# Kernel optimization log

Measured on AMD Instinct MI355X. Metric: run time of the kernel, lower is better.

The kernel has to match this reference:

```python
import jax, jax.numpy as jnp
import numpy as np

GAMMA = 0.7
ALPHA = 1.0
EPS = 1e-6

def setup_inputs() -> dict:
    key = jax.random.key(0)
    k1, k2 = jax.random.split(key)
    x = jax.random.normal(k1, (1, 4096, 1024), dtype=jnp.float32)
    attn = jax.random.uniform(k2, (1, 4096, 4096), dtype=jnp.float32)
    return {"x": x, "attn": attn, "layer_idx": 10, "total_layers": 12}


def reference(x, attn, layer_idx, total_layers):
    B, N, D = x.shape  # module's masking/cat logic requires B == 1
    if layer_idx < GAMMA * total_layers:
        return x

    # --- spatial autocorrelation score s ---
    a = x.mean(axis=-1)                                            # [B,N]
    z = (a - a.mean(1, keepdims=True)) / (a.std(1, ddof=1, keepdims=True) + EPS)
    # diag(z z^T * W) == z^2 * diag(W): skip the O(N^2) outer product
    I_l = z * z * jnp.diagonal(attn, axis1=-2, axis2=-1)           # [B,N]
    s = (I_l - I_l.mean(1, keepdims=True)) / (I_l.std(1, ddof=1, keepdims=True) + EPS)

    # --- threshold (torch.median returns the LOWER middle for even N) ---
    mu_s = s.mean(1, keepdims=True)
    abs_med = jnp.sort(jnp.abs(s), axis=1)[:, (N - 1) // 2][:, None]
    lb = ALPHA * (mu_s - abs_med)
    ub = ALPHA * (mu_s + abs_med)
    mask_A = (s < lb) | (s > ub)                                   # [B,N]

    xb = x[0]
    mA = mask_A[0]
    idx = jnp.arange(N)
    n_A = mA.sum()

    # compact A tokens to the front preserving original order
    orderA = jnp.argsort(~mA, stable=True)
    tokA = xb[orderA]                    # first n_A rows are tokens_A, rest are B tokens (masked later)
    mid = n_A // 2
    n2 = n_A - mid                       # number of A2 tokens

    # A1[i] = tokA[i] (valid i < mid); A2[j] = tokA[mid + j] (valid j < n2)
    A2 = jnp.take(tokA, jnp.clip(mid + idx, 0, N - 1), axis=0)     # [N,D] padded
    validA1 = idx < mid
    validA2 = idx < n2

    sim = tokA @ A2.T                                              # [N,N]
    sim = jnp.where(validA2[None, :], sim, -jnp.inf)
    matches = jnp.argmax(sim, axis=1)                              # [N]
    merged = 0.5 * (tokA + A2[matches])
    merged = jnp.where(validA1[:, None], merged, 0.0)              # rows >= mid zeroed

    # residual A2 tokens (not matched by any valid A1 row), compacted and zero-padded
    drop_idx = jnp.where(validA1, matches, N)                      # OOB index dropped
    matched = jnp.zeros(N, bool).at[drop_idx].set(True, mode='drop')
    resid_valid = validA2 & ~matched
    orderR = jnp.argsort(~resid_valid, stable=True)
    residual = jnp.where(resid_valid[orderR][:, None], A2[orderR], 0.0)  # [N,D]

    # B tokens compacted, then merged tokens appended, zero pad to N
    n_B = N - n_A
    orderB = jnp.argsort(mA, stable=True)
    tokB = jnp.where((idx < n_B)[:, None], xb[orderB], 0.0)        # [N,D]
    shift = jnp.clip(idx - n_B, 0, N - 1)
    in_merged = ((idx >= n_B) & (idx < n_B + mid)).astype(xb.dtype)[:, None]
    out = (tokB + in_merged * merged[shift])[None]                 # [1,N,D]
    return out, residual
```

## Files before the change

### kernel.cpp

```cpp
#include <hip/hip_runtime.h>

#define N 4096
#define D 1024
#define EPSF 1e-6f

typedef _Float16 f16;
typedef f16 f16x8 __attribute__((ext_vector_type(8)));
typedef float f32x4 __attribute__((ext_vector_type(4)));
typedef unsigned long long u64;

struct WS {
  int n_A, mid, n2, n_B, n_resid, pad[3];
  float a[N];
  int A1idx[N];
  int A2idx[N];
  int Bidx[N];
  int matches[N];
  int residIdx[N];
  u64 bestKey[2048];
};

__device__ __forceinline__ u64 packKey(float v, int j) {
  unsigned u = __float_as_uint(v);
  unsigned m = (u & 0x80000000u) ? ~u : (u | 0x80000000u);
  return ((u64)m << 32) | (unsigned)(~(unsigned)j);
}

__global__ __launch_bounds__(256) void k_prep(const float* __restrict__ x, WS* ws) {
  int row = blockIdx.x;
  int t = threadIdx.x;
  float4 v = ((const float4*)(x + (size_t)row * D))[t];
  float sm = v.x + v.y + v.z + v.w;
  for (int o = 32; o; o >>= 1) sm += __shfl_down(sm, o, 64);
  __shared__ float w[4];
  if ((t & 63) == 0) w[t >> 6] = sm;
  __syncthreads();
  if (t == 0) ws->a[row] = (w[0] + w[1] + w[2] + w[3]) * (1.0f / D);
}

__global__ __launch_bounds__(1024) void k_mask(const float* __restrict__ attn, WS* ws) {
  __shared__ double dred[16], dred2[16];
  __shared__ float bcast[2];
  __shared__ int hist[256];
  __shared__ int wsum[16];
  __shared__ unsigned sPrefix;
  __shared__ int sRank;
  int tid = threadIdx.x;
  int lane = tid & 63, wv = tid >> 6;

  ws->bestKey[tid] = 0ull;
  ws->bestKey[tid + 1024] = 0ull;

  float av[4];
  double s = 0.0, s2 = 0.0;
  #pragma unroll
  for (int q = 0; q < 4; q++) {
    float f = ws->a[tid * 4 + q];
    av[q] = f; s += f; s2 += (double)f * f;
  }
  for (int o = 32; o; o >>= 1) { s += __shfl_down(s, o, 64); s2 += __shfl_down(s2, o, 64); }
  if (lane == 0) { dred[wv] = s; dred2[wv] = s2; }
  __syncthreads();
  if (tid == 0) {
    double t1 = 0, t2 = 0;
    for (int i = 0; i < 16; i++) { t1 += dred[i]; t2 += dred2[i]; }
    bcast[0] = (float)(t1 / N);
    bcast[1] = (float)sqrt((t2 - t1 * t1 / N) / (N - 1));
  }
  __syncthreads();
  float meanA = bcast[0], stdA = bcast[1];

  float il[4];
  s = 0.0; s2 = 0.0;
  #pragma unroll
  for (int q = 0; q < 4; q++) {
    int i = tid * 4 + q;
    float z = (av[q] - meanA) / (stdA + EPSF);
    float I = z * z * attn[(size_t)i * N + i];
    il[q] = I; s += I; s2 += (double)I * I;
  }
  for (int o = 32; o; o >>= 1) { s += __shfl_down(s, o, 64); s2 += __shfl_down(s2, o, 64); }
  __syncthreads();
  if (lane == 0) { dred[wv] = s; dred2[wv] = s2; }
  __syncthreads();
  if (tid == 0) {
    double t1 = 0, t2 = 0;
    for (int i = 0; i < 16; i++) { t1 += dred[i]; t2 += dred2[i]; }
    bcast[0] = (float)(t1 / N);
    bcast[1] = (float)sqrt((t2 - t1 * t1 / N) / (N - 1));
    sPrefix = 0u; sRank = (N - 1) / 2;
  }
  __syncthreads();
  float meanI = bcast[0], stdI = bcast[1];

  float sv[4]; unsigned ab[4];
  #pragma unroll
  for (int q = 0; q < 4; q++) {
    float sval = (il[q] - meanI) / (stdI + EPSF);
    sv[q] = sval;
    ab[q] = __float_as_uint(fabsf(sval));
  }

  for (int p = 3; p >= 0; p--) {
    if (tid < 256) hist[tid] = 0;
    __syncthreads();
    unsigned pre = sPrefix;
    int rk = sRank;
    int sh = p * 8;
    unsigned mHi = (p == 3) ? 0u : (0xFFFFFFFFu << (sh + 8));
    #pragma unroll
    for (int q = 0; q < 4; q++)
      if ((ab[q] & mHi) == pre) atomicAdd(&hist[(ab[q] >> sh) & 255], 1);
    __syncthreads();
    int v = (tid < 256) ? hist[tid] : 0;
    int inc = v;
    #pragma unroll
    for (int o = 1; o < 64; o <<= 1) { int u = __shfl_up(inc, o, 64); if (lane >= o) inc += u; }
    if (lane == 63) wsum[wv] = inc;
    __syncthreads();
    if (tid < 16) {
      int t = wsum[tid];
      #pragma unroll
      for (int o = 1; o < 16; o <<= 1) { int u = __shfl_up(t, o, 64); if (tid >= o) t += u; }
      wsum[tid] = t;
    }
    __syncthreads();
    int incl = (wv ? wsum[wv - 1] : 0) + inc;
    int E = incl - v;
    if (tid < 256 && v && rk >= E && rk < E + v) {
      sPrefix = pre | ((unsigned)tid << sh);
      sRank = rk - E;
    }
    __syncthreads();
  }
  float med = __uint_as_float(sPrefix);

  int msk[4], loc[4]; int tot = 0;
  #pragma unroll
  for (int q = 0; q < 4; q++) {
    bool m = fabsf(sv[q]) > med;
    msk[q] = m; loc[q] = tot; tot += (int)m;
  }
  int inc = tot;
  #pragma unroll
  for (int o = 1; o < 64; o <<= 1) { int u = __shfl_up(inc, o, 64); if (lane >= o) inc += u; }
  if (lane == 63) wsum[wv] = inc;
  __syncthreads();
  if (tid < 16) {
    int t = wsum[tid];
    #pragma unroll
    for (int o = 1; o < 16; o <<= 1) { int u = __shfl_up(t, o, 64); if (tid >= o) t += u; }
    wsum[tid] = t;
  }
  __syncthreads();
  int nA = wsum[15];
  int base = (wv ? wsum[wv - 1] : 0) + inc - tot;
  int midl = nA >> 1;
  #pragma unroll
  for (int q = 0; q < 4; q++) {
    int i = tid * 4 + q;
    int r = base + loc[q];
    if (msk[q]) {
      if (r < midl) ws->A1idx[r] = i; else ws->A2idx[r - midl] = i;
    } else {
      ws->Bidx[i - r] = i;
    }
  }
  if (tid == 0) { ws->n_A = nA; ws->mid = midl; ws->n2 = nA - midl; ws->n_B = N - nA; }
}

__global__ __launch_bounds__(256) void k_gemm(const float* __restrict__ x, WS* ws) {
  const int mid = ws->mid, n2 = ws->n2;
  const int bi = blockIdx.y, bj = blockIdx.x;
  if (bi * 64 >= mid || bj * 64 >= n2) return;

  __shared__ f16 lds[2][4][64 * 64];

  const int tid = threadIdx.x;
  const int lane = tid & 63;
  const int wid = tid >> 6;
  const int wr = wid >> 1, wc = wid & 1;

  const int srow = tid >> 2;
  const int sc = tid & 3;
  int ra = bi * 64 + srow; if (ra > mid - 1) ra = mid - 1;
  int rb = bj * 64 + srow; if (rb > n2 - 1) rb = n2 - 1;
  const float* pA = x + (size_t)ws->A1idx[ra] * D;
  const float* pB = x + (size_t)ws->A2idx[rb] * D;

  const int wo0 = srow * 64 + (((sc * 2) ^ (srow & 7)) * 8);
  const int wo1 = srow * 64 + (((sc * 2 + 1) ^ (srow & 7)) * 8);

  float fav[16], fbv[16];
  auto LOAD = [&](int t) {
    const float4* qa = (const float4*)(pA + t * 64 + sc * 16);
    const float4* qb = (const float4*)(pB + t * 64 + sc * 16);
    #pragma unroll
    for (int q = 0; q < 4; q++) {
      float4 va = qa[q], vb = qb[q];
      fav[q * 4 + 0] = va.x; fav[q * 4 + 1] = va.y; fav[q * 4 + 2] = va.z; fav[q * 4 + 3] = va.w;
      fbv[q * 4 + 0] = vb.x; fbv[q * 4 + 1] = vb.y; fbv[q * 4 + 2] = vb.z; fbv[q * 4 + 3] = vb.w;
    }
  };
  auto STORE = [&](int buf) {
    f16x8 ah0, ah1, al0, al1, bh0, bh1, bl0, bl1;
    #pragma unroll
    for (int e = 0; e < 8; e++) {
      f16 h;
      h = (f16)fav[e];     ah0[e] = h; al0[e] = (f16)(fav[e] - (float)h);
      h = (f16)fav[8 + e]; ah1[e] = h; al1[e] = (f16)(fav[8 + e] - (float)h);
      h = (f16)fbv[e];     bh0[e] = h; bl0[e] = (f16)(fbv[e] - (float)h);
      h = (f16)fbv[8 + e]; bh1[e] = h; bl1[e] = (f16)(fbv[8 + e] - (float)h);
    }
    *(f16x8*)&lds[buf][0][wo0] = ah0; *(f16x8*)&lds[buf][0][wo1] = ah1;
    *(f16x8*)&lds[buf][1][wo0] = al0; *(f16x8*)&lds[buf][1][wo1] = al1;
    *(f16x8*)&lds[buf][2][wo0] = bh0; *(f16x8*)&lds[buf][2][wo1] = bh1;
    *(f16x8*)&lds[buf][3][wo0] = bl0; *(f16x8*)&lds[buf][3][wo1] = bl1;
  };

  const int colg = lane & 15, rowg = lane >> 4;
  const int ma0 = wr * 32 + colg, ma1 = ma0 + 16;
  const int mb0 = wc * 32 + colg, mb1 = mb0 + 16;

  f32x4 zero = {0.0f, 0.0f, 0.0f, 0.0f};
  f32x4 acc[2][2];
  acc[0][0] = zero; acc[0][1] = zero; acc[1][0] = zero; acc[1][1] = zero;

#define FRAG(buf, t4, row, g) \
  (*(const f16x8*)&lds[buf][t4][(row) * 64 + ((((g) ^ ((row) & 7))) * 8)])

  LOAD(0);
  STORE(0);
  __syncthreads();
  for (int t16 = 0; t16 < 16; t16++) {
    int buf = t16 & 1;
    if (t16 < 15) LOAD(t16 + 1);
    #pragma unroll
    for (int ks = 0; ks < 2; ks++) {
      int gk = ks * 4 + rowg;
      f16x8 ah0 = FRAG(buf, 0, ma0, gk), ah1 = FRAG(buf, 0, ma1, gk);
      f16x8 al0 = FRAG(buf, 1, ma0, gk), al1 = FRAG(buf, 1, ma1, gk);
      f16x8 bh0 = FRAG(buf, 2, mb0, gk), bh1 = FRAG(buf, 2, mb1, gk);
      f16x8 bl0 = FRAG(buf, 3, mb0, gk), bl1 = FRAG(buf, 3, mb1, gk);
      acc[0][0] = __builtin_amdgcn_mfma_f32_16x16x32_f16(ah0, bh0, acc[0][0], 0, 0, 0);
      acc[0][0] = __builtin_amdgcn_mfma_f32_16x16x32_f16(ah0, bl0, acc[0][0], 0, 0, 0);
      acc[0][0] = __builtin_amdgcn_mfma_f32_16x16x32_f16(al0, bh0, acc[0][0], 0, 0, 0);
      acc[0][1] = __builtin_amdgcn_mfma_f32_16x16x32_f16(ah0, bh1, acc[0][1], 0, 0, 0);
      acc[0][1] = __builtin_amdgcn_mfma_f32_16x16x32_f16(ah0, bl1, acc[0][1], 0, 0, 0);
      acc[0][1] = __builtin_amdgcn_mfma_f32_16x16x32_f16(al0, bh1, acc[0][1], 0, 0, 0);
      acc[1][0] = __builtin_amdgcn_mfma_f32_16x16x32_f16(ah1, bh0, acc[1][0], 0, 0, 0);
      acc[1][0] = __builtin_amdgcn_mfma_f32_16x16x32_f16(ah1, bl0, acc[1][0], 0, 0, 0);
      acc[1][0] = __builtin_amdgcn_mfma_f32_16x16x32_f16(al1, bh0, acc[1][0], 0, 0, 0);
      acc[1][1] = __builtin_amdgcn_mfma_f32_16x16x32_f16(ah1, bh1, acc[1][1], 0, 0, 0);
      acc[1][1] = __builtin_amdgcn_mfma_f32_16x16x32_f16(ah1, bl1, acc[1][1], 0, 0, 0);
      acc[1][1] = __builtin_amdgcn_mfma_f32_16x16x32_f16(al1, bh1, acc[1][1], 0, 0, 0);
    }
    if (t16 < 15) {
      __syncthreads();
      STORE(buf ^ 1);
      __syncthreads();
    }
  }
#undef FRAG

  #pragma unroll
  for (int mi = 0; mi < 2; mi++) {
    #pragma unroll
    for (int i = 0; i < 4; i++) {
      int grow = bi * 64 + wr * 32 + mi * 16 + rowg * 4 + i;
      u64 key = 0;
      #pragma unroll
      for (int ni = 0; ni < 2; ni++) {
        int gcol = bj * 64 + wc * 32 + ni * 16 + colg;
        if (gcol < n2) {
          u64 k2 = packKey(acc[mi][ni][i], gcol);
          if (k2 > key) key = k2;
        }
      }
      #pragma unroll
      for (int m = 8; m; m >>= 1) {
        u64 o = (u64)__shfl_xor((long long)key, m, 64);
        if (o > key) key = o;
      }
      if (colg == 0 && grow < mid) atomicMax(&ws->bestKey[grow], key);
    }
  }
}

__global__ __launch_bounds__(1024) void k_match(WS* ws) {
  __shared__ int flag[N];
  __shared__ int wsum[16];
  int tid = threadIdx.x;
  int lane = tid & 63, wv = tid >> 6;
  int mid = ws->mid, n2 = ws->n2;
  #pragma unroll
  for (int q = 0; q < 4; q++) flag[tid * 4 + q] = 0;
  __syncthreads();
  #pragma unroll
  for (int q = 0; q < 2; q++) {
    int r = tid + q * 1024;
    if (r < mid) {
      int j = (int)(~(unsigned)(ws->bestKey[r] & 0xffffffffull));
      ws->matches[r] = j;
      flag[j] = 1;
    }
  }
  __syncthreads();
  int v[4], loc[4]; int tot = 0;
  #pragma unroll
  for (int q = 0; q < 4; q++) {
    int j = tid * 4 + q;
    bool val = (j < n2) && (flag[j] == 0);
    v[q] = val; loc[q] = tot; tot += (int)val;
  }
  int inc = tot;
  #pragma unroll
  for (int o = 1; o < 64; o <<= 1) { int u = __shfl_up(inc, o, 64); if (lane >= o) inc += u; }
  if (lane == 63) wsum[wv] = inc;
  __syncthreads();
  if (tid < 16) {
    int t = wsum[tid];
    #pragma unroll
    for (int o = 1; o < 16; o <<= 1) { int u = __shfl_up(t, o, 64); if (tid >= o) t += u; }
    wsum[tid] = t;
  }
  __syncthreads();
  int base = (wv ? wsum[wv - 1] : 0) + inc - tot;
  #pragma unroll
  for (int q = 0; q < 4; q++)
    if (v[q]) ws->residIdx[base + loc[q]] = ws->A2idx[tid * 4 + q];
  if (tid == 0) ws->n_resid = wsum[15];
}

__global__ __launch_bounds__(256) void k_write(const float* __restrict__ x,
                                               float* __restrict__ out, WS* ws) {
  int r = blockIdx.x;
  int t = threadIdx.x;
  int n_B = ws->n_B, mid = ws->mid, n_resid = ws->n_resid;
  float4 res = make_float4(0.f, 0.f, 0.f, 0.f);
  if (r < N) {
    if (r < n_B) {
      res = ((const float4*)(x + (size_t)ws->Bidx[r] * D))[t];
    } else if (r < n_B + mid) {
      int m = r - n_B;
      float4 v1 = ((const float4*)(x + (size_t)ws->A1idx[m] * D))[t];
      float4 v2 = ((const float4*)(x + (size_t)ws->A2idx[ws->matches[m]] * D))[t];
      res = make_float4(0.5f * (v1.x + v2.x), 0.5f * (v1.y + v2.y),
                        0.5f * (v1.z + v2.z), 0.5f * (v1.w + v2.w));
    }
  } else {
    int k = r - N;
    if (k < n_resid) {
      res = ((const float4*)(x + (size_t)ws->residIdx[k] * D))[t];
    }
  }
  ((float4*)(out + (size_t)r * D))[t] = res;
}

extern "C" void kernel_launch(void* const* d_in, const int* in_sizes, int n_in,
                              void* d_out, int out_size, void* d_ws, size_t ws_size,
                              hipStream_t stream) {
  const float* x = (const float*)d_in[0];
  const float* attn = (const float*)d_in[1];
  float* out = (float*)d_out;
  WS* ws = (WS*)d_ws;

  k_prep<<<N, 256, 0, stream>>>(x, ws);
  k_mask<<<1, 1024, 0, stream>>>(attn, ws);
  dim3 g(32, 32);
  k_gemm<<<g, 256, 0, stream>>>(x, ws);
  k_match<<<1, 1024, 0, stream>>>(ws);
  k_write<<<2 * N, 256, 0, stream>>>(x, out, ws);
}
```

Measured before the change: 68.93 us.

## Precompute fp16 hi/lo split in prep and use split-K direct-load GEMM

The prep kernel now writes fp16 hi/lo splits of x into the output buffer, used as scratch. The GEMM no longer converts fp32 to fp16 pairs per tile through LDS. The GEMM switches to 32x32 tiles with two waves, each covering half of K. Fragments load directly from global memory without LDS staging, the two halves are combined through shared memory, and blocks are remapped with an XCD-aware swizzle. This removes repeated conversion work and LDS barriers but gives up LDS reuse, relying on cache for the repeated row reads. It also depends on k_write later overwriting the scratch region of the output.

Result: slower. 74.05 us (+7.4%).

```diff
diff --git a/kernel.cpp b/kernel.cpp
--- a/kernel.cpp
+++ b/kernel.cpp
@@ -6,6 +6,7 @@
 
 typedef _Float16 f16;
 typedef f16 f16x8 __attribute__((ext_vector_type(8)));
+typedef f16 f16x4 __attribute__((ext_vector_type(4)));
 typedef float f32x4 __attribute__((ext_vector_type(4)));
 typedef unsigned long long u64;
 
@@ -26,10 +27,22 @@
   return ((u64)m << 32) | (unsigned)(~(unsigned)j);
 }
 
-__global__ __launch_bounds__(256) void k_prep(const float* __restrict__ x, WS* ws) {
+__global__ __launch_bounds__(256) void k_prep(const float* __restrict__ x,
+                                              f16* __restrict__ hi,
+                                              f16* __restrict__ lo, WS* ws) {
   int row = blockIdx.x;
   int t = threadIdx.x;
   float4 v = ((const float4*)(x + (size_t)row * D))[t];
+  float vv[4] = {v.x, v.y, v.z, v.w};
+  f16x4 h, l;
+  #pragma unroll
+  for (int q = 0; q < 4; q++) {
+    f16 hq = (f16)vv[q];
+    h[q] = hq;
+    l[q] = (f16)(vv[q] - (float)hq);
+  }
+  *(f16x4*)(hi + (size_t)row * D + t * 4) = h;
+  *(f16x4*)(lo + (size_t)row * D + t * 4) = l;
   float sm = v.x + v.y + v.z + v.w;
   for (int o = 32; o; o >>= 1) sm += __shfl_down(sm, o, 64);
   __shared__ float w[4];
@@ -169,120 +182,111 @@
   if (tid == 0) { ws->n_A = nA; ws->mid = midl; ws->n2 = nA - midl; ws->n_B = N - nA; }
 }
 
-__global__ __launch_bounds__(256) void k_gemm(const float* __restrict__ x, WS* ws) {
+__global__ __launch_bounds__(128) void k_gemm(const f16* __restrict__ hi,
+                                              const f16* __restrict__ lo, WS* ws) {
   const int mid = ws->mid, n2 = ws->n2;
-  const int bi = blockIdx.y, bj = blockIdx.x;
-  if (bi * 64 >= mid || bj * 64 >= n2) return;
-
-  __shared__ f16 lds[2][4][64 * 64];
+  int L = blockIdx.x;
+  int local = L >> 3;
+  int bj = ((L & 7) << 2) | (local >> 5);
+  int bi = local & 31;
+  if (bi * 32 >= mid || bj * 32 >= n2) return;
+
+  __shared__ float comb[64][17];
 
   const int tid = threadIdx.x;
+  const int w = tid >> 6;
   const int lane = tid & 63;
-  const int wid = tid >> 6;
-  const int wr = wid >> 1, wc = wid & 1;
-
-  const int srow = tid >> 2;
-  const int sc = tid & 3;
-  int ra = bi * 64 + srow; if (ra > mid - 1) ra = mid - 1;
-  int rb = bj * 64 + srow; if (rb > n2 - 1) rb = n2 - 1;
-  const float* pA = x + (size_t)ws->A1idx[ra] * D;
-  const float* pB = x + (size_t)ws->A2idx[rb] * D;
-
-  const int wo0 = srow * 64 + (((sc * 2) ^ (srow & 7)) * 8);
-  const int wo1 = srow * 64 + (((sc * 2 + 1) ^ (srow & 7)) * 8);
-
-  float fav[16], fbv[16];
-  auto LOAD = [&](int t) {
-    const float4* qa = (const float4*)(pA + t * 64 + sc * 16);
-    const float4* qb = (const float4*)(pB + t * 64 + sc * 16);
-    #pragma unroll
-    for (int q = 0; q < 4; q++) {
-      float4 va = qa[q], vb = qb[q];
-      fav[q * 4 + 0] = va.x; fav[q * 4 + 1] = va.y; fav[q * 4 + 2] = va.z; fav[q * 4 + 3] = va.w;
-      fbv[q * 4 + 0] = vb.x; fbv[q * 4 + 1] = vb.y; fbv[q * 4 + 2] = vb.z; fbv[q * 4 + 3] = vb.w;
-    }
-  };
-  auto STORE = [&](int buf) {
-    f16x8 ah0, ah1, al0, al1, bh0, bh1, bl0, bl1;
-    #pragma unroll
-    for (int e = 0; e < 8; e++) {
-      f16 h;
-      h = (f16)fav[e];     ah0[e] = h; al0[e] = (f16)(fav[e] - (float)h);
-      h = (f16)fav[8 + e]; ah1[e] = h; al1[e] = (f16)(fav[8 + e] - (float)h);
-      h = (f16)fbv[e];     bh0[e] = h; bl0[e] = (f16)(fbv[e] - (float)h);
-      h = (f16)fbv[8 + e]; bh1[e] = h; bl1[e] = (f16)(fbv[8 + e] - (float)h);
-    }
-    *(f16x8*)&lds[buf][0][wo0] = ah0; *(f16x8*)&lds[buf][0][wo1] = ah1;
-    *(f16x8*)&lds[buf][1][wo0] = al0; *(f16x8*)&lds[buf][1][wo1] = al1;
-    *(f16x8*)&lds[buf][2][wo0] = bh0; *(f16x8*)&lds[buf][2][wo1] = bh1;
-    *(f16x8*)&lds[buf][3][wo0] = bl0; *(f16x8*)&lds[buf][3][wo1] = bl1;
-  };
-
   const int colg = lane & 15, rowg = lane >> 4;
-  const int ma0 = wr * 32 + colg, ma1 = ma0 + 16;
-  const int mb0 = wc * 32 + colg, mb1 = mb0 + 16;
-
-  f32x4 zero = {0.0f, 0.0f, 0.0f, 0.0f};
-  f32x4 acc[2][2];
-  acc[0][0] = zero; acc[0][1] = zero; acc[1][0] = zero; acc[1][1] = zero;
-
-#define FRAG(buf, t4, row, g) \
-  (*(const f16x8*)&lds[buf][t4][(row) * 64 + ((((g) ^ ((row) & 7))) * 8)])
-
-  LOAD(0);
-  STORE(0);
-  __syncthreads();
-  for (int t16 = 0; t16 < 16; t16++) {
-    int buf = t16 & 1;
-    if (t16 < 15) LOAD(t16 + 1);
-    #pragma unroll
-    for (int ks = 0; ks < 2; ks++) {
-      int gk = ks * 4 + rowg;
-      f16x8 ah0 = FRAG(buf, 0, ma0, gk), ah1 = FRAG(buf, 0, ma1, gk);
-      f16x8 al0 = FRAG(buf, 1, ma0, gk), al1 = FRAG(buf, 1, ma1, gk);
-      f16x8 bh0 = FRAG(buf, 2, mb0, gk), bh1 = FRAG(buf, 2, mb1, gk);
-      f16x8 bl0 = FRAG(buf, 3, mb0, gk), bl1 = FRAG(buf, 3, mb1, gk);
-      acc[0][0] = __builtin_amdgcn_mfma_f32_16x16x32_f16(ah0, bh0, acc[0][0], 0, 0, 0);
-      acc[0][0] = __builtin_amdgcn_mfma_f32_16x16x32_f16(ah0, bl0, acc[0][0], 0, 0, 0);
-      acc[0][0] = __builtin_amdgcn_mfma_f32_16x16x32_f16(al0, bh0, acc[0][0], 0, 0, 0);
-      acc[0][1] = __builtin_amdgcn_mfma_f32_16x16x32_f16(ah0, bh1, acc[0][1], 0, 0, 0);
-      acc[0][1] = __builtin_amdgcn_mfma_f32_16x16x32_f16(ah0, bl1, acc[0][1], 0, 0, 0);
-      acc[0][1] = __builtin_amdgcn_mfma_f32_16x16x32_f16(al0, bh1, acc[0][1], 0, 0, 0);
-      acc[1][0] = __builtin_amdgcn_mfma_f32_16x16x32_f16(ah1, bh0, acc[1][0], 0, 0, 0);
-      acc[1][0] = __builtin_amdgcn_mfma_f32_16x16x32_f16(ah1, bl0, acc[1][0], 0, 0, 0);
-      acc[1][0] = __builtin_amdgcn_mfma_f32_16x16x32_f16(al1, bh0, acc[1][0], 0, 0, 0);
-      acc[1][1] = __builtin_amdgcn_mfma_f32_16x16x32_f16(ah1, bh1, acc[1][1], 0, 0, 0);
-      acc[1][1] = __builtin_amdgcn_mfma_f32_16x16x32_f16(ah1, bl1, acc[1][1], 0, 0, 0);
-      acc[1][1] = __builtin_amdgcn_mfma_f32_16x16x32_f16(al1, bh1, acc[1][1], 0, 0, 0);
-    }
-    if (t16 < 15) {
-      __syncthreads();
-      STORE(buf ^ 1);
-      __syncthreads();
-    }
-  }
-#undef FRAG
-
-  #pragma unroll
-  for (int mi = 0; mi < 2; mi++) {
-    #pragma unroll
-    for (int i = 0; i < 4; i++) {
-      int grow = bi * 64 + wr * 32 + mi * 16 + rowg * 4 + i;
-      u64 key = 0;
+
+  int ar0 = bi * 32 + colg;      if (ar0 > mid - 1) ar0 = mid - 1;
+  int ar1 = ar0 + 16;            if (ar1 > mid - 1) ar1 = mid - 1;
+  int br0 = bj * 32 + colg;      if (br0 > n2 - 1) br0 = n2 - 1;
+  int br1 = br0 + 16;            if (br1 > n2 - 1) br1 = n2 - 1;
+  const size_t off = (size_t)w * 1024 + rowg * 16;
+  const char* pAh0 = (const char*)hi + (size_t)ws->A1idx[ar0] * 2048 + off;
+  const char* pAh1 = (const char*)hi + (size_t)ws->A1idx[ar1] * 2048 + off;
+  const char* pAl0 = (const char*)lo + (size_t)ws->A1idx[ar0] * 2048 + off;
+  const char* pAl1 = (const char*)lo + (size_t)ws->A1idx[ar1] * 2048 + off;
+  const char* pBh0 = (const char*)hi + (size_t)ws->A2idx[br0] * 2048 + off;
+  const char* pBh1 = (const char*)hi + (size_t)ws->A2idx[br1] * 2048 + off;
+  const char* pBl0 = (const char*)lo + (size_t)ws->A2idx[br0] * 2048 + off;
+  const char* pBl1 = (const char*)lo + (size_t)ws->A2idx[br1] * 2048 + off;
+
+  f32x4 zero = {0.f, 0.f, 0.f, 0.f};
+  f32x4 hh[2][2], hl[2][2], lh[2][2];
+  #pragma unroll
+  for (int i = 0; i < 2; i++)
+    #pragma unroll
+    for (int j = 0; j < 2; j++) { hh[i][j] = zero; hl[i][j] = zero; lh[i][j] = zero; }
+
+  #pragma unroll
+  for (int t = 0; t < 16; t++) {
+    const int o = t * 64;
+    f16x8 ah0 = *(const f16x8*)(pAh0 + o);
+    f16x8 ah1 = *(const f16x8*)(pAh1 + o);
+    f16x8 al0 = *(const f16x8*)(pAl0 + o);
+    f16x8 al1 = *(const f16x8*)(pAl1 + o);
+    f16x8 bh0 = *(const f16x8*)(pBh0 + o);
+    f16x8 bh1 = *(const f16x8*)(pBh1 + o);
+    f16x8 bl0 = *(const f16x8*)(pBl0 + o);
+    f16x8 bl1 = *(const f16x8*)(pBl1 + o);
+    hh[0][0] = __builtin_amdgcn_mfma_f32_16x16x32_f16(ah0, bh0, hh[0][0], 0, 0, 0);
+    hh[0][1] = __builtin_amdgcn_mfma_f32_16x16x32_f16(ah0, bh1, hh[0][1], 0, 0, 0);
+    hh[1][0] = __builtin_amdgcn_mfma_f32_16x16x32_f16(ah1, bh0, hh[1][0], 0, 0, 0);
+    hh[1][1] = __builtin_amdgcn_mfma_f32_16x16x32_f16(ah1, bh1, hh[1][1], 0, 0, 0);
+    hl[0][0] = __builtin_amdgcn_mfma_f32_16x16x32_f16(ah0, bl0, hl[0][0], 0, 0, 0);
+    hl[0][1] = __builtin_amdgcn_mfma_f32_16x16x32_f16(ah0, bl1, hl[0][1], 0, 0, 0);
+    hl[1][0] = __builtin_amdgcn_mfma_f32_16x16x32_f16(ah1, bl0, hl[1][0], 0, 0, 0);
+    hl[1][1] = __builtin_amdgcn_mfma_f32_16x16x32_f16(ah1, bl1, hl[1][1], 0, 0, 0);
+    lh[0][0] = __builtin_amdgcn_mfma_f32_16x16x32_f16(al0, bh0, lh[0][0], 0, 0, 0);
+    lh[0][1] = __builtin_amdgcn_mfma_f32_16x16x32_f16(al0, bh1, lh[0][1], 0, 0, 0);
+    lh[1][0] = __builtin_amdgcn_mfma_f32_16x16x32_f16(al1, bh0, lh[1][0], 0, 0, 0);
+    lh[1][1] = __builtin_amdgcn_mfma_f32_16x16x32_f16(al1, bh1, lh[1][1], 0, 0, 0);
+  }
+
+  f32x4 s[2][2];
+  #pragma unroll
+  for (int i = 0; i < 2; i++)
+    #pragma unroll
+    for (int j = 0; j < 2; j++) s[i][j] = (hh[i][j] + hl[i][j]) + lh[i][j];
+
+  if (w == 1) {
+    #pragma unroll
+    for (int i = 0; i < 2; i++)
       #pragma unroll
-      for (int ni = 0; ni < 2; ni++) {
-        int gcol = bj * 64 + wc * 32 + ni * 16 + colg;
-        if (gcol < n2) {
-          u64 k2 = packKey(acc[mi][ni][i], gcol);
-          if (k2 > key) key = k2;
+      for (int j = 0; j < 2; j++)
+        #pragma unroll
+        for (int r = 0; r < 4; r++) comb[lane][i * 8 + j * 4 + r] = s[i][j][r];
+  }
+  __syncthreads();
+  if (w == 0) {
+    #pragma unroll
+    for (int i = 0; i < 2; i++)
+      #pragma unroll
+      for (int j = 0; j < 2; j++)
+        #pragma unroll
+        for (int r = 0; r < 4; r++) s[i][j][r] += comb[lane][i * 8 + j * 4 + r];
+    #pragma unroll
+    for (int mi = 0; mi < 2; mi++) {
+      #pragma unroll
+      for (int r = 0; r < 4; r++) {
+        int grow = bi * 32 + mi * 16 + rowg * 4 + r;
+        u64 key = 0;
+        #pragma unroll
+        for (int ni = 0; ni < 2; ni++) {
+          int gcol = bj * 32 + ni * 16 + colg;
+          if (gcol < n2) {
+            u64 k2 = packKey(s[mi][ni][r], gcol);
+            if (k2 > key) key = k2;
+          }
         }
+        #pragma unroll
+        for (int m = 8; m; m >>= 1) {
+          u64 o = (u64)__shfl_xor((long long)key, m, 64);
+          if (o > key) key = o;
+        }
+        if (colg == 0 && grow < mid && key) atomicMax(&ws->bestKey[grow], key);
       }
-      #pragma unroll
-      for (int m = 8; m; m >>= 1) {
-        u64 o = (u64)__shfl_xor((long long)key, m, 64);
-        if (o > key) key = o;
-      }
-      if (colg == 0 && grow < mid) atomicMax(&ws->bestKey[grow], key);
     }
   }
 }
@@ -364,11 +368,12 @@
   const float* attn = (const float*)d_in[1];
   float* out = (float*)d_out;
   WS* ws = (WS*)d_ws;
-
-  k_prep<<<N, 256, 0, stream>>>(x, ws);
+  f16* hi = (f16*)d_out;
+  f16* lo = hi + (size_t)N * D;
+
+  k_prep<<<N, 256, 0, stream>>>(x, hi, lo, ws);
   k_mask<<<1, 1024, 0, stream>>>(attn, ws);
-  dim3 g(32, 32);
-  k_gemm<<<g, 256, 0, stream>>>(x, ws);
+  k_gemm<<<1024, 128, 0, stream>>>(hi, lo, ws);
   k_match<<<1, 1024, 0, stream>>>(ws);
   k_write<<<2 * N, 256, 0, stream>>>(x, out, ws);
 }
```

## Pre-pack gathered A tokens into fp16 hi/lo planes before GEMM

Applied to the files above, without the earlier changes.

Adds a k_pack kernel that gathers the A1/A2 rows and splits them once into fp16 hi and lo planes, stored in scratch space borrowed from the output buffer. The GEMM then loads the pre-split fp16 tiles straight into shared memory with one plane per wave, so the fp32 loads and hi/lo conversion are no longer repeated for every tile pair. The grid is also remapped to a swizzled 1D order, presumably to improve cache locality, and atomics with empty keys are skipped. The cost is an extra kernel launch plus writing and re-reading about 16 MB of packed data, and correctness depends on k_write overwriting the borrowed output region afterwards.

Result: faster. 64.07 us (-7.1%).

```diff
diff --git a/kernel.cpp b/kernel.cpp
--- a/kernel.cpp
+++ b/kernel.cpp
@@ -6,6 +6,7 @@
 
 typedef _Float16 f16;
 typedef f16 f16x8 __attribute__((ext_vector_type(8)));
+typedef f16 f16x4 __attribute__((ext_vector_type(4)));
 typedef float f32x4 __attribute__((ext_vector_type(4)));
 typedef unsigned long long u64;
 
@@ -169,9 +170,45 @@
   if (tid == 0) { ws->n_A = nA; ws->mid = midl; ws->n2 = nA - midl; ws->n_B = N - nA; }
 }
 
-__global__ __launch_bounds__(256) void k_gemm(const float* __restrict__ x, WS* ws) {
+__global__ __launch_bounds__(256) void k_pack(const float* __restrict__ x,
+                                              f16* __restrict__ PAhi, f16* __restrict__ PAlo,
+                                              f16* __restrict__ PBhi, f16* __restrict__ PBlo,
+                                              WS* ws) {
+  int b = blockIdx.x, t = threadIdx.x;
+  const float* src;
+  f16 *dh, *dl;
+  if (b < 2048) {
+    if (b >= ws->mid) return;
+    src = x + (size_t)ws->A1idx[b] * D;
+    dh = PAhi + (size_t)b * D; dl = PAlo + (size_t)b * D;
+  } else {
+    int j = b - 2048;
+    if (j >= ws->n2) return;
+    src = x + (size_t)ws->A2idx[j] * D;
+    dh = PBhi + (size_t)j * D; dl = PBlo + (size_t)j * D;
+  }
+  float4 v = ((const float4*)src)[t];
+  float vv[4] = {v.x, v.y, v.z, v.w};
+  f16x4 h, l;
+  #pragma unroll
+  for (int q = 0; q < 4; q++) {
+    f16 hq = (f16)vv[q];
+    h[q] = hq;
+    l[q] = (f16)(vv[q] - (float)hq);
+  }
+  *(f16x4*)(dh + t * 4) = h;
+  *(f16x4*)(dl + t * 4) = l;
+}
+
+__global__ __launch_bounds__(256) void k_gemm(const f16* __restrict__ PAhi,
+                                              const f16* __restrict__ PAlo,
+                                              const f16* __restrict__ PBhi,
+                                              const f16* __restrict__ PBlo, WS* ws) {
   const int mid = ws->mid, n2 = ws->n2;
-  const int bi = blockIdx.y, bj = blockIdx.x;
+  int L = blockIdx.x;
+  int local = L >> 3;
+  int bj = ((L & 7) << 2) | (local >> 5);
+  int bi = local & 31;
   if (bi * 64 >= mid || bj * 64 >= n2) return;
 
   __shared__ f16 lds[2][4][64 * 64];
@@ -181,48 +218,33 @@
   const int wid = tid >> 6;
   const int wr = wid >> 1, wc = wid & 1;
 
-  const int srow = tid >> 2;
-  const int sc = tid & 3;
-  int ra = bi * 64 + srow; if (ra > mid - 1) ra = mid - 1;
-  int rb = bj * 64 + srow; if (rb > n2 - 1) rb = n2 - 1;
-  const float* pA = x + (size_t)ws->A1idx[ra] * D;
-  const float* pB = x + (size_t)ws->A2idx[rb] * D;
-
-  const int wo0 = srow * 64 + (((sc * 2) ^ (srow & 7)) * 8);
-  const int wo1 = srow * 64 + (((sc * 2 + 1) ^ (srow & 7)) * 8);
-
-  float fav[16], fbv[16];
+  const f16* plane = (wid == 0) ? PAhi : (wid == 1) ? PAlo : (wid == 2) ? PBhi : PBlo;
+  const int pbase = (wid < 2) ? bi * 64 : bj * 64;
+  const int pmax = ((wid < 2) ? mid : n2) - 1;
+  const int src_g = (lane & 7) ^ (lane >> 3);
+  const char* rp[8];
+  #pragma unroll
+  for (int i = 0; i < 8; i++) {
+    int row = pbase + i * 8 + (lane >> 3);
+    if (row > pmax) row = pmax;
+    rp[i] = (const char*)(plane + (size_t)row * D) + src_g * 16;
+  }
+
+  f16x8 pr[8];
   auto LOAD = [&](int t) {
-    const float4* qa = (const float4*)(pA + t * 64 + sc * 16);
-    const float4* qb = (const float4*)(pB + t * 64 + sc * 16);
-    #pragma unroll
-    for (int q = 0; q < 4; q++) {
-      float4 va = qa[q], vb = qb[q];
-      fav[q * 4 + 0] = va.x; fav[q * 4 + 1] = va.y; fav[q * 4 + 2] = va.z; fav[q * 4 + 3] = va.w;
-      fbv[q * 4 + 0] = vb.x; fbv[q * 4 + 1] = vb.y; fbv[q * 4 + 2] = vb.z; fbv[q * 4 + 3] = vb.w;
-    }
+    #pragma unroll
+    for (int i = 0; i < 8; i++) pr[i] = *(const f16x8*)(rp[i] + t * 128);
   };
   auto STORE = [&](int buf) {
-    f16x8 ah0, ah1, al0, al1, bh0, bh1, bl0, bl1;
-    #pragma unroll
-    for (int e = 0; e < 8; e++) {
-      f16 h;
-      h = (f16)fav[e];     ah0[e] = h; al0[e] = (f16)(fav[e] - (float)h);
-      h = (f16)fav[8 + e]; ah1[e] = h; al1[e] = (f16)(fav[8 + e] - (float)h);
-      h = (f16)fbv[e];     bh0[e] = h; bl0[e] = (f16)(fbv[e] - (float)h);
-      h = (f16)fbv[8 + e]; bh1[e] = h; bl1[e] = (f16)(fbv[8 + e] - (float)h);
-    }
-    *(f16x8*)&lds[buf][0][wo0] = ah0; *(f16x8*)&lds[buf][0][wo1] = ah1;
-    *(f16x8*)&lds[buf][1][wo0] = al0; *(f16x8*)&lds[buf][1][wo1] = al1;
-    *(f16x8*)&lds[buf][2][wo0] = bh0; *(f16x8*)&lds[buf][2][wo1] = bh1;
-    *(f16x8*)&lds[buf][3][wo0] = bl0; *(f16x8*)&lds[buf][3][wo1] = bl1;
+    #pragma unroll
+    for (int i = 0; i < 8; i++) *(f16x8*)&lds[buf][wid][i * 512 + lane * 8] = pr[i];
   };
 
   const int colg = lane & 15, rowg = lane >> 4;
   const int ma0 = wr * 32 + colg, ma1 = ma0 + 16;
   const int mb0 = wc * 32 + colg, mb1 = mb0 + 16;
 
-  f32x4 zero = {0.0f, 0.0f, 0.0f, 0.0f};
+  f32x4 zero = {0.f, 0.f, 0.f, 0.f};
   f32x4 acc[2][2];
   acc[0][0] = zero; acc[0][1] = zero; acc[1][0] = zero; acc[1][1] = zero;
 
@@ -282,7 +304,7 @@
         u64 o = (u64)__shfl_xor((long long)key, m, 64);
         if (o > key) key = o;
       }
-      if (colg == 0 && grow < mid) atomicMax(&ws->bestKey[grow], key);
+      if (colg == 0 && grow < mid && key) atomicMax(&ws->bestKey[grow], key);
     }
   }
 }
@@ -364,11 +386,15 @@
   const float* attn = (const float*)d_in[1];
   float* out = (float*)d_out;
   WS* ws = (WS*)d_ws;
+  f16* PAhi = (f16*)d_out;
+  f16* PAlo = PAhi + (size_t)2048 * D;
+  f16* PBhi = PAlo + (size_t)2048 * D;
+  f16* PBlo = PBhi + (size_t)2048 * D;
 
   k_prep<<<N, 256, 0, stream>>>(x, ws);
   k_mask<<<1, 1024, 0, stream>>>(attn, ws);
-  dim3 g(32, 32);
-  k_gemm<<<g, 256, 0, stream>>>(x, ws);
+  k_pack<<<4096, 256, 0, stream>>>(x, PAhi, PAlo, PBhi, PBlo, ws);
+  k_gemm<<<1024, 256, 0, stream>>>(PAhi, PAlo, PBhi, PBlo, ws);
   k_match<<<1, 1024, 0, stream>>>(ws);
   k_write<<<2 * N, 256, 0, stream>>>(x, out, ws);
 }
```
